# Performance work log

Measured on AMD Instinct MI355X. Metric: run time of the kernel, lower is better.

## Reference

```python
import jax, jax.numpy as jnp
import numpy as np

NEG_SLOPE = 0.2  # PyG GATConv default


def leaky_relu(v):
    return jnp.where(v >= 0, v, NEG_SLOPE * v)


def gat_conv(x, W, a_src, a_dst, b, src, dst, n_nodes):
    # x: [N, Fin], W: [Fin, Fout], a_src/a_dst/b: [Fout]
    h = x @ W                               # [N, Fout]
    alpha_src = h @ a_src                   # [N]
    alpha_dst = h @ a_dst                   # [N]
    e = leaky_relu(alpha_src[src] + alpha_dst[dst])          # [E]
    m = jax.ops.segment_max(e, dst, num_segments=n_nodes)    # [N] (self-loops => every node has >=1 edge)
    p = jnp.exp(e - m[dst])                                   # [E]
    s = jax.ops.segment_sum(p, dst, num_segments=n_nodes)     # [N]
    coef = p / s[dst]                                          # [E]
    out = jax.ops.segment_sum(coef[:, None] * h[src], dst, num_segments=n_nodes)
    return out + b


def setup_inputs() -> dict:
    key = jax.random.key(0)
    ks = jax.random.split(key, 20)
    N, E, DIN, DH, DOUT, G = 50000, 800000, 128, 256, 2, 512
    x = jax.random.normal(ks[0], (N, DIN), dtype=jnp.float32)
    edge_index = jax.random.randint(ks[1], (2, E), 0, N, dtype=jnp.int64)
    batch = jnp.sort(jax.random.randint(ks[2], (N,), 0, G, dtype=jnp.int64))

    def lin(k, fin, fout):
        return jax.random.normal(k, (fin, fout), dtype=jnp.float32) * (1.0 / np.sqrt(fin))

    def att(k, f):
        return jax.random.normal(k, (f,), dtype=jnp.float32) * (1.0 / np.sqrt(f))

    return {
        "x": x, "edge_index": edge_index, "batch": batch,
        "W1": lin(ks[3], DIN, DH), "as1": att(ks[4], DH), "ad1": att(ks[5], DH), "b1": jnp.zeros((DH,), jnp.float32),
        "W2": lin(ks[6], DH, DH),  "as2": att(ks[7], DH), "ad2": att(ks[8], DH), "b2": jnp.zeros((DH,), jnp.float32),
        "W3": lin(ks[9], DH, DH),  "as3": att(ks[10], DH), "ad3": att(ks[11], DH), "b3": jnp.zeros((DH,), jnp.float32),
        "Wfc": lin(ks[12], DH, DOUT), "bfc": jnp.zeros((DOUT,), jnp.float32),
    }


def reference(x, edge_index, batch, W1, as1, ad1, b1, W2, as2, ad2, b2, W3, as3, ad3, b3, Wfc, bfc):
    N = x.shape[0]
    G = 512  # number of graphs (static)
    # add self-loops (PyG GATConv default add_self_loops=True)
    loops = jnp.arange(N, dtype=edge_index.dtype)
    src = jnp.concatenate([edge_index[0], loops])
    dst = jnp.concatenate([edge_index[1], loops])

    h = jax.nn.relu(gat_conv(x, W1, as1, ad1, b1, src, dst, N))
    h = jax.nn.relu(gat_conv(h, W2, as2, ad2, b2, src, dst, N))
    h = jax.nn.relu(gat_conv(h, W3, as3, ad3, b3, src, dst, N))

    # global mean pool over graphs
    sums = jax.ops.segment_sum(h, batch, num_segments=G)                 # [G, DH]
    counts = jax.ops.segment_sum(jnp.ones((N,), h.dtype), batch, num_segments=G)
    pooled = sums / jnp.maximum(counts, 1.0)[:, None]

    logits = pooled @ Wfc + bfc                                           # [G, DOUT]
    return jax.nn.softmax(logits, axis=1)
```

## Files before the change

### kernel.cpp

```cpp
#include <hip/hip_runtime.h>
#include <hip/hip_bf16.h>

typedef short short8 __attribute__((ext_vector_type(8)));
typedef float floatx4 __attribute__((ext_vector_type(4)));
typedef unsigned short ushort_t;
typedef unsigned short ushort4v __attribute__((ext_vector_type(4)));

__device__ __forceinline__ ushort_t f2bf(float v) {
    __hip_bfloat16 h = __float2bfloat16(v);
    return *(ushort_t*)&h;
}
__device__ __forceinline__ float bf2f(ushort_t u) {
    return __uint_as_float(((unsigned)u) << 16);
}
__device__ __forceinline__ float4 ldh4(const ushort_t* p) {
    ushort4v u = *(const ushort4v*)p;
    return make_float4(bf2f(u.x), bf2f(u.y), bf2f(u.z), bf2f(u.w));
}

__global__ __launch_bounds__(256) void wsplit_kernel(const float* __restrict__ W,
                                                     ushort_t* __restrict__ Bthi,
                                                     ushort_t* __restrict__ Btlo, int K) {
    int idx = blockIdx.x * 256 + threadIdx.x;
    if (idx >= K * 256) return;
    int n = idx & 255, k = idx >> 8;
    float v = W[(size_t)k * 256 + n];
    ushort_t h = f2bf(v);
    float r = v - bf2f(h);
    Bthi[(size_t)n * K + k] = h;
    Btlo[(size_t)n * K + k] = f2bf(r);
}

#define ASTR 40
#define BSTR 56
__global__ __launch_bounds__(256, 2) void gemm_mfma(const float* __restrict__ A,
                                                    const ushort_t* __restrict__ Bthi,
                                                    const ushort_t* __restrict__ Btlo,
                                                    ushort_t* __restrict__ Hb,
                                                    const float* __restrict__ a_src,
                                                    const float* __restrict__ a_dst,
                                                    float* __restrict__ asrc_out,
                                                    float* __restrict__ adst_out,
                                                    int N, int K) {
    __shared__ ushort_t Ahi[128 * ASTR];
    __shared__ ushort_t Alo[128 * ASTR];
    __shared__ ushort_t Bhi[128 * BSTR];
    __shared__ ushort_t Blo[128 * BSTR];

    const int tid = threadIdx.x;
    const int wave = tid >> 6, lane = tid & 63;
    const int wr = wave & 1, wc = wave >> 1;
    const int q = lane >> 4, l15 = lane & 15;
    const int rowBase = blockIdx.x * 128;
    const int colBase = blockIdx.y * 128;

    floatx4 acc[4][4];
#pragma unroll
    for (int i = 0; i < 4; ++i)
#pragma unroll
        for (int j = 0; j < 4; ++j) acc[i][j] = (floatx4)0.f;

    const int a_row = tid >> 1;
    const int a_k0  = (tid & 1) * 16;
    const int b_n   = tid >> 1;
    const int b_k0  = (tid & 1) * 16;

    for (int kc = 0; kc < K; kc += 32) {
        {
            int grow = rowBase + a_row;
            float v[16];
            if (grow < N) {
                const float* ap = A + (size_t)grow * K + kc + a_k0;
                float4 t0 = *(const float4*)(ap + 0);
                float4 t1 = *(const float4*)(ap + 4);
                float4 t2 = *(const float4*)(ap + 8);
                float4 t3 = *(const float4*)(ap + 12);
                v[0]=t0.x; v[1]=t0.y; v[2]=t0.z; v[3]=t0.w;
                v[4]=t1.x; v[5]=t1.y; v[6]=t1.z; v[7]=t1.w;
                v[8]=t2.x; v[9]=t2.y; v[10]=t2.z; v[11]=t2.w;
                v[12]=t3.x; v[13]=t3.y; v[14]=t3.z; v[15]=t3.w;
            } else {
#pragma unroll
                for (int i = 0; i < 16; ++i) v[i] = 0.f;
            }
            int base = a_row * ASTR + a_k0;
#pragma unroll
            for (int i = 0; i < 16; i += 2) {
                ushort_t h0 = f2bf(v[i]),     h1 = f2bf(v[i + 1]);
                ushort_t l0 = f2bf(v[i] - bf2f(h0));
                ushort_t l1 = f2bf(v[i + 1] - bf2f(h1));
                *(uint*)&Ahi[base + i] = (uint)h0 | ((uint)h1 << 16);
                *(uint*)&Alo[base + i] = (uint)l0 | ((uint)l1 << 16);
            }
        }
        {
            const ushort_t* bh = Bthi + (size_t)(colBase + b_n) * K + kc + b_k0;
            const ushort_t* bl = Btlo + (size_t)(colBase + b_n) * K + kc + b_k0;
            int base = b_n * BSTR + b_k0;
            *(short8*)&Bhi[base + 0] = *(const short8*)(bh + 0);
            *(short8*)&Bhi[base + 8] = *(const short8*)(bh + 8);
            *(short8*)&Blo[base + 0] = *(const short8*)(bl + 0);
            *(short8*)&Blo[base + 8] = *(const short8*)(bl + 8);
        }
        __syncthreads();

        short8 afh[4], afl[4], bfh[4], bfl[4];
#pragma unroll
        for (int mt = 0; mt < 4; ++mt) {
            int r = wr * 64 + mt * 16 + l15;
            afh[mt] = *(short8*)&Ahi[r * ASTR + q * 8];
            afl[mt] = *(short8*)&Alo[r * ASTR + q * 8];
        }
#pragma unroll
        for (int nt = 0; nt < 4; ++nt) {
            int n = wc * 64 + nt * 16 + l15;
            bfh[nt] = *(short8*)&Bhi[n * BSTR + q * 8];
            bfl[nt] = *(short8*)&Blo[n * BSTR + q * 8];
        }
#pragma unroll
        for (int mt = 0; mt < 4; ++mt)
#pragma unroll
            for (int nt = 0; nt < 4; ++nt) {
                acc[mt][nt] = __builtin_amdgcn_mfma_f32_16x16x32_bf16(afh[mt], bfh[nt], acc[mt][nt], 0, 0, 0);
                acc[mt][nt] = __builtin_amdgcn_mfma_f32_16x16x32_bf16(afh[mt], bfl[nt], acc[mt][nt], 0, 0, 0);
                acc[mt][nt] = __builtin_amdgcn_mfma_f32_16x16x32_bf16(afl[mt], bfh[nt], acc[mt][nt], 0, 0, 0);
            }
        __syncthreads();
    }

    float asv[4], adv[4];
#pragma unroll
    for (int nt = 0; nt < 4; ++nt) {
        int n = colBase + wc * 64 + nt * 16 + l15;
        asv[nt] = a_src[n];
        adv[nt] = a_dst[n];
    }
#pragma unroll
    for (int mt = 0; mt < 4; ++mt) {
#pragma unroll
        for (int reg = 0; reg < 4; ++reg) {
            int grow = rowBase + wr * 64 + mt * 16 + q * 4 + reg;
            float p1 = acc[mt][0][reg] * asv[0] + acc[mt][1][reg] * asv[1] +
                       acc[mt][2][reg] * asv[2] + acc[mt][3][reg] * asv[3];
            float p2 = acc[mt][0][reg] * adv[0] + acc[mt][1][reg] * adv[1] +
                       acc[mt][2][reg] * adv[2] + acc[mt][3][reg] * adv[3];
            if (grow < N) {
                ushort_t* crow = Hb + (size_t)grow * 256 + colBase + wc * 64 + l15;
#pragma unroll
                for (int nt = 0; nt < 4; ++nt) crow[nt * 16] = f2bf(acc[mt][nt][reg]);
            }
#pragma unroll
            for (int off = 1; off < 16; off <<= 1) {
                p1 += __shfl_xor(p1, off, 64);
                p2 += __shfl_xor(p2, off, 64);
            }
            if (l15 == 0 && grow < N) {
                atomicAdd(&asrc_out[grow], p1);
                atomicAdd(&adst_out[grow], p2);
            }
        }
    }
}

__global__ __launch_bounds__(256) void count_kernel(const int* __restrict__ edst,
                                                    int* __restrict__ deg, int E) {
    int i = blockIdx.x * 256 + threadIdx.x;
    if (i < E) atomicAdd(&deg[edst[i]], 1);
}

__global__ __launch_bounds__(256) void scan1_kernel(const int* __restrict__ deg,
                                                    int* __restrict__ excl,
                                                    int* __restrict__ bsum, int N) {
    __shared__ int tmp[256];
    int tid = threadIdx.x;
    int i = blockIdx.x * 256 + tid;
    int v = (i < N) ? deg[i] : 0;
    tmp[tid] = v;
    __syncthreads();
    for (int off = 1; off < 256; off <<= 1) {
        int t = (tid >= off) ? tmp[tid - off] : 0;
        __syncthreads();
        tmp[tid] += t;
        __syncthreads();
    }
    if (i < N) excl[i] = tmp[tid] - v;
    if (tid == 255) bsum[blockIdx.x] = tmp[255];
}

__global__ __launch_bounds__(256) void scan2_kernel(int* __restrict__ bsum, int nb) {
    __shared__ int tmp[256];
    int tid = threadIdx.x;
    int v = (tid < nb) ? bsum[tid] : 0;
    tmp[tid] = v;
    __syncthreads();
    for (int off = 1; off < 256; off <<= 1) {
        int t = (tid >= off) ? tmp[tid - off] : 0;
        __syncthreads();
        tmp[tid] += t;
        __syncthreads();
    }
    if (tid < nb) bsum[tid] = tmp[tid] - v;
}

__global__ __launch_bounds__(256) void scan3_kernel(const int* __restrict__ excl,
                                                    const int* __restrict__ bsum,
                                                    int* __restrict__ rowptr,
                                                    int* __restrict__ cursor,
                                                    int N, int E) {
    int i = blockIdx.x * 256 + threadIdx.x;
    if (i < N) {
        int v = excl[i] + bsum[blockIdx.x];
        rowptr[i] = v;
        cursor[i] = v;
    }
    if (i == 0) rowptr[N] = E;
}

__global__ __launch_bounds__(256) void scatter_kernel(const int* __restrict__ esrc,
                                                      const int* __restrict__ edst,
                                                      int* __restrict__ cursor,
                                                      int* __restrict__ csr_src, int E) {
    int i = blockIdx.x * 256 + threadIdx.x;
    if (i < E) {
        int d = edst[i];
        int pos = atomicAdd(&cursor[d], 1);
        csr_src[pos] = esrc[i];
    }
}

__global__ __launch_bounds__(256) void gat_fused_kernel(const ushort_t* __restrict__ hb,
                                                        const float* __restrict__ asrc,
                                                        const float* __restrict__ adst,
                                                        const int* __restrict__ rowptr,
                                                        const int* __restrict__ csr_src,
                                                        const float* __restrict__ bias,
                                                        float* __restrict__ out, int N) {
    int wave = threadIdx.x >> 6;
    int lane = threadIdx.x & 63;
    int d = blockIdx.x * 4 + wave;
    if (d >= N) return;

    float ad = adst[d];
    float es = asrc[d] + ad;
    es = es >= 0.f ? es : 0.2f * es;
    float m = es;
    float s = 1.0f;
    float4 acc = ldh4(hb + (size_t)d * 256 + lane * 4);

    int beg = rowptr[d], end = rowptr[d + 1];
    for (int base = beg; base < end; base += 64) {
        int cnt = min(64, end - base);
        int srci = 0;
        float e = -1e30f;
        if (lane < cnt) {
            srci = csr_src[base + lane];
            float v = asrc[srci] + ad;
            e = v >= 0.f ? v : 0.2f * v;
        }
        float cm = e;
#pragma unroll
        for (int off = 32; off > 0; off >>= 1) cm = fmaxf(cm, __shfl_xor(cm, off, 64));
        float mnew = fmaxf(m, cm);
        float scale = __expf(m - mnew);
        s *= scale;
        acc.x *= scale; acc.y *= scale; acc.z *= scale; acc.w *= scale;
        m = mnew;

        int j = 0;
        for (; j + 4 <= cnt; j += 4) {
            float e0 = __shfl(e, j, 64),     e1 = __shfl(e, j + 1, 64);
            float e2 = __shfl(e, j + 2, 64), e3 = __shfl(e, j + 3, 64);
            int s0 = __shfl(srci, j, 64),     s1i = __shfl(srci, j + 1, 64);
            int s2i = __shfl(srci, j + 2, 64), s3i = __shfl(srci, j + 3, 64);
            float4 hv0 = ldh4(hb + (size_t)s0 * 256 + lane * 4);
            float4 hv1 = ldh4(hb + (size_t)s1i * 256 + lane * 4);
            float4 hv2 = ldh4(hb + (size_t)s2i * 256 + lane * 4);
            float4 hv3 = ldh4(hb + (size_t)s3i * 256 + lane * 4);
            float p0 = __expf(e0 - m), p1 = __expf(e1 - m);
            float p2 = __expf(e2 - m), p3 = __expf(e3 - m);
            s += p0 + p1 + p2 + p3;
            acc.x += p0 * hv0.x + p1 * hv1.x + p2 * hv2.x + p3 * hv3.x;
            acc.y += p0 * hv0.y + p1 * hv1.y + p2 * hv2.y + p3 * hv3.y;
            acc.z += p0 * hv0.z + p1 * hv1.z + p2 * hv2.z + p3 * hv3.z;
            acc.w += p0 * hv0.w + p1 * hv1.w + p2 * hv2.w + p3 * hv3.w;
        }
        for (; j < cnt; ++j) {
            float ej = __shfl(e, j, 64);
            int sj = __shfl(srci, j, 64);
            float p = __expf(ej - m);
            float4 hv = ldh4(hb + (size_t)sj * 256 + lane * 4);
            s += p;
            acc.x += p * hv.x; acc.y += p * hv.y; acc.z += p * hv.z; acc.w += p * hv.w;
        }
    }
    float inv = 1.0f / s;
    float4 bv = *(const float4*)(bias + lane * 4);
    float4 o;
    o.x = fmaxf(acc.x * inv + bv.x, 0.f);
    o.y = fmaxf(acc.y * inv + bv.y, 0.f);
    o.z = fmaxf(acc.z * inv + bv.z, 0.f);
    o.w = fmaxf(acc.w * inv + bv.w, 0.f);
    *(float4*)(out + (size_t)d * 256 + lane * 4) = o;
}

__device__ __forceinline__ int lower_bound_i(const int* __restrict__ a, int n, int v) {
    int lo = 0, hi = n;
    while (lo < hi) {
        int mid = (lo + hi) >> 1;
        if (a[mid] < v) lo = mid + 1; else hi = mid;
    }
    return lo;
}

__global__ __launch_bounds__(256) void pool_fc_kernel(const float* __restrict__ h,
                                                      const int* __restrict__ batch,
                                                      int N,
                                                      const float* __restrict__ Wfc,
                                                      const float* __restrict__ bfc,
                                                      float* __restrict__ out) {
    __shared__ float red0[256];
    __shared__ float red1[256];
    int g = blockIdx.x;
    int c = threadIdx.x;
    int beg = lower_bound_i(batch, N, g);
    int end = lower_bound_i(batch, N, g + 1);
    float sum = 0.f;
    for (int n = beg; n < end; ++n) sum += h[(size_t)n * 256 + c];
    float cnt = (float)(end - beg);
    float v = sum / fmaxf(cnt, 1.0f);
    red0[c] = v * Wfc[c * 2 + 0];
    red1[c] = v * Wfc[c * 2 + 1];
    __syncthreads();
    for (int off = 128; off > 0; off >>= 1) {
        if (c < off) {
            red0[c] += red0[c + off];
            red1[c] += red1[c + off];
        }
        __syncthreads();
    }
    if (c == 0) {
        float l0 = red0[0] + bfc[0];
        float l1 = red1[0] + bfc[1];
        float mx = fmaxf(l0, l1);
        float e0 = expf(l0 - mx), e1 = expf(l1 - mx);
        float s = e0 + e1;
        out[g * 2 + 0] = e0 / s;
        out[g * 2 + 1] = e1 / s;
    }
}

extern "C" void kernel_launch(void* const* d_in, const int* in_sizes, int n_in,
                              void* d_out, int out_size, void* d_ws, size_t ws_size,
                              hipStream_t stream) {
    const float* x    = (const float*)d_in[0];
    const int*   eidx = (const int*)d_in[1];
    const int*   batch= (const int*)d_in[2];
    const float* Wl[3]  = {(const float*)d_in[3], (const float*)d_in[7],  (const float*)d_in[11]};
    const float* asl[3] = {(const float*)d_in[4], (const float*)d_in[8],  (const float*)d_in[12]};
    const float* adl[3] = {(const float*)d_in[5], (const float*)d_in[9],  (const float*)d_in[13]};
    const float* bl[3]  = {(const float*)d_in[6], (const float*)d_in[10], (const float*)d_in[14]};
    const float* Wfc = (const float*)d_in[15];
    const float* bfc = (const float*)d_in[16];
    float* out = (float*)d_out;

    const int N  = in_sizes[2];
    const int E  = in_sizes[1] / 2;
    const int DH = 256;
    const int G  = 512;
    const int* esrc = eidx;
    const int* edst = eidx + E;

    char* ws = (char*)d_ws;
    size_t off = 0;
    const size_t featBytes = (size_t)N * DH * sizeof(float);
    ushort_t* hb     = (ushort_t*)(ws + off); off += (size_t)N * DH * sizeof(ushort_t);
    float*    bufB   = (float*)(ws + off); off += featBytes;
    float*    asrc   = (float*)(ws + off); off += (size_t)N * sizeof(float);
    float*    adst   = (float*)(ws + off); off += (size_t)N * sizeof(float);
    int*      deg    = (int*)(ws + off);   off += (size_t)N * sizeof(int);
    int*      excl   = (int*)(ws + off);   off += (size_t)N * sizeof(int);
    int*      rowptr = (int*)(ws + off);   off += (size_t)(N + 1) * sizeof(int);
    int*      cursor = (int*)(ws + off);   off += (size_t)N * sizeof(int);
    int*      bsum   = (int*)(ws + off);   off += 1024;
    int*      csrsrc = (int*)(ws + off);   off += (size_t)E * sizeof(int);
    ushort_t* Bthi   = (ushort_t*)(ws + off); off += (size_t)256 * 256 * sizeof(ushort_t);
    ushort_t* Btlo   = (ushort_t*)(ws + off); off += (size_t)256 * 256 * sizeof(ushort_t);

    const int nbN = (N + 255) / 256;

    hipMemsetAsync(deg, 0, (size_t)N * sizeof(int), stream);
    count_kernel<<<(E + 255) / 256, 256, 0, stream>>>(edst, deg, E);
    scan1_kernel<<<nbN, 256, 0, stream>>>(deg, excl, bsum, N);
    scan2_kernel<<<1, 256, 0, stream>>>(bsum, nbN);
    scan3_kernel<<<nbN, 256, 0, stream>>>(excl, bsum, rowptr, cursor, N, E);
    scatter_kernel<<<(E + 255) / 256, 256, 0, stream>>>(esrc, edst, cursor, csrsrc, E);

    for (int layer = 0; layer < 3; ++layer) {
        const float* in = (layer == 0) ? x : bufB;
        const int K = (layer == 0) ? 128 : 256;

        hipMemsetAsync(asrc, 0, 2 * (size_t)N * sizeof(float), stream);
        wsplit_kernel<<<K, 256, 0, stream>>>(Wl[layer], Bthi, Btlo, K);

        dim3 ggrid((N + 127) / 128, 2);
        gemm_mfma<<<ggrid, 256, 0, stream>>>(in, Bthi, Btlo, hb,
                                             asl[layer], adl[layer], asrc, adst, N, K);

        gat_fused_kernel<<<(N + 3) / 4, 256, 0, stream>>>(hb, asrc, adst, rowptr, csrsrc,
                                                          bl[layer], bufB, N);
    }

    pool_fc_kernel<<<G, 256, 0, stream>>>(bufB, batch, N, Wfc, bfc, out);
}
```

Measured before the change: 534.5 us.

## Pre-split activations into bf16 hi/lo planes outside the GEMM

The GAT aggregation kernel now writes its output directly as bf16 hi/lo pairs, and a new pre-pass splits x the same way, so the GEMM loads ready-made hi/lo tiles instead of converting fp32 per tile. LDS padding is unified to a single stride and the occupancy hint is raised to 4 blocks per CU. Pooling reads and sums the two planes. This removes conversion ALU work from the GEMM inner loop while keeping the same bytes per feature. The cost is an extra split kernel and a possible LDS bank-conflict change from the new stride.

```diff
diff --git a/kernel.cpp b/kernel.cpp
--- a/kernel.cpp
+++ b/kernel.cpp
@@ -16,6 +16,17 @@
 __device__ __forceinline__ float4 ldh4(const ushort_t* p) {
     ushort4v u = *(const ushort4v*)p;
     return make_float4(bf2f(u.x), bf2f(u.y), bf2f(u.z), bf2f(u.w));
+}
+
+__global__ __launch_bounds__(256) void xsplit_kernel(const float* __restrict__ X,
+                                                     ushort_t* __restrict__ Xhi,
+                                                     ushort_t* __restrict__ Xlo, int total) {
+    int idx = blockIdx.x * 256 + threadIdx.x;
+    if (idx >= total) return;
+    float v = X[idx];
+    ushort_t h = f2bf(v);
+    Xhi[idx] = h;
+    Xlo[idx] = f2bf(v - bf2f(h));
 }
 
 __global__ __launch_bounds__(256) void wsplit_kernel(const float* __restrict__ W,
@@ -31,9 +42,9 @@
     Btlo[(size_t)n * K + k] = f2bf(r);
 }
 
-#define ASTR 40
-#define BSTR 56
-__global__ __launch_bounds__(256, 2) void gemm_mfma(const float* __restrict__ A,
+#define LSTR 36
+__global__ __launch_bounds__(256, 4) void gemm_mfma(const ushort_t* __restrict__ Ahi_g,
+                                                    const ushort_t* __restrict__ Alo_g,
                                                     const ushort_t* __restrict__ Bthi,
                                                     const ushort_t* __restrict__ Btlo,
                                                     ushort_t* __restrict__ Hb,
@@ -42,10 +53,10 @@
                                                     float* __restrict__ asrc_out,
                                                     float* __restrict__ adst_out,
                                                     int N, int K) {
-    __shared__ ushort_t Ahi[128 * ASTR];
-    __shared__ ushort_t Alo[128 * ASTR];
-    __shared__ ushort_t Bhi[128 * BSTR];
-    __shared__ ushort_t Blo[128 * BSTR];
+    __shared__ ushort_t Ahi[128 * LSTR];
+    __shared__ ushort_t Alo[128 * LSTR];
+    __shared__ ushort_t Bhi[128 * LSTR];
+    __shared__ ushort_t Blo[128 * LSTR];
 
     const int tid = threadIdx.x;
     const int wave = tid >> 6, lane = tid & 63;
@@ -62,41 +73,30 @@
 
     const int a_row = tid >> 1;
     const int a_k0  = (tid & 1) * 16;
-    const int b_n   = tid >> 1;
-    const int b_k0  = (tid & 1) * 16;
+    const short8 zero8 = (short8)0;
 
     for (int kc = 0; kc < K; kc += 32) {
         {
             int grow = rowBase + a_row;
-            float v[16];
+            int base = a_row * LSTR + a_k0;
             if (grow < N) {
-                const float* ap = A + (size_t)grow * K + kc + a_k0;
-                float4 t0 = *(const float4*)(ap + 0);
-                float4 t1 = *(const float4*)(ap + 4);
-                float4 t2 = *(const float4*)(ap + 8);
-                float4 t3 = *(const float4*)(ap + 12);
-                v[0]=t0.x; v[1]=t0.y; v[2]=t0.z; v[3]=t0.w;
-                v[4]=t1.x; v[5]=t1.y; v[6]=t1.z; v[7]=t1.w;
-                v[8]=t2.x; v[9]=t2.y; v[10]=t2.z; v[11]=t2.w;
-                v[12]=t3.x; v[13]=t3.y; v[14]=t3.z; v[15]=t3.w;
+                const ushort_t* ah = Ahi_g + (size_t)grow * K + kc + a_k0;
+                const ushort_t* al = Alo_g + (size_t)grow * K + kc + a_k0;
+                *(short8*)&Ahi[base + 0] = *(const short8*)(ah + 0);
+                *(short8*)&Ahi[base + 8] = *(const short8*)(ah + 8);
+                *(short8*)&Alo[base + 0] = *(const short8*)(al + 0);
+                *(short8*)&Alo[base + 8] = *(const short8*)(al + 8);
             } else {
-#pragma unroll
-                for (int i = 0; i < 16; ++i) v[i] = 0.f;
+                *(short8*)&Ahi[base + 0] = zero8;
+                *(short8*)&Ahi[base + 8] = zero8;
+                *(short8*)&Alo[base + 0] = zero8;
+                *(short8*)&Alo[base + 8] = zero8;
             }
-            int base = a_row * ASTR + a_k0;
-#pragma unroll
-            for (int i = 0; i < 16; i += 2) {
-                ushort_t h0 = f2bf(v[i]),     h1 = f2bf(v[i + 1]);
-                ushort_t l0 = f2bf(v[i] - bf2f(h0));
-                ushort_t l1 = f2bf(v[i + 1] - bf2f(h1));
-                *(uint*)&Ahi[base + i] = (uint)h0 | ((uint)h1 << 16);
-                *(uint*)&Alo[base + i] = (uint)l0 | ((uint)l1 << 16);
-            }
         }
         {
-            const ushort_t* bh = Bthi + (size_t)(colBase + b_n) * K + kc + b_k0;
-            const ushort_t* bl = Btlo + (size_t)(colBase + b_n) * K + kc + b_k0;
-            int base = b_n * BSTR + b_k0;
+            const ushort_t* bh = Bthi + (size_t)(colBase + a_row) * K + kc + a_k0;
+            const ushort_t* bl = Btlo + (size_t)(colBase + a_row) * K + kc + a_k0;
+            int base = a_row * LSTR + a_k0;
             *(short8*)&Bhi[base + 0] = *(const short8*)(bh + 0);
             *(short8*)&Bhi[base + 8] = *(const short8*)(bh + 8);
             *(short8*)&Blo[base + 0] = *(const short8*)(bl + 0);
@@ -108,14 +108,14 @@
 #pragma unroll
         for (int mt = 0; mt < 4; ++mt) {
             int r = wr * 64 + mt * 16 + l15;
-            afh[mt] = *(short8*)&Ahi[r * ASTR + q * 8];
-            afl[mt] = *(short8*)&Alo[r * ASTR + q * 8];
+            afh[mt] = *(short8*)&Ahi[r * LSTR + q * 8];
+            afl[mt] = *(short8*)&Alo[r * LSTR + q * 8];
         }
 #pragma unroll
         for (int nt = 0; nt < 4; ++nt) {
             int n = wc * 64 + nt * 16 + l15;
-            bfh[nt] = *(short8*)&Bhi[n * BSTR + q * 8];
-            bfl[nt] = *(short8*)&Blo[n * BSTR + q * 8];
+            bfh[nt] = *(short8*)&Bhi[n * LSTR + q * 8];
+            bfl[nt] = *(short8*)&Blo[n * LSTR + q * 8];
         }
 #pragma unroll
         for (int mt = 0; mt < 4; ++mt)
@@ -234,7 +234,8 @@
                                                         const int* __restrict__ rowptr,
                                                         const int* __restrict__ csr_src,
                                                         const float* __restrict__ bias,
-                                                        float* __restrict__ out, int N) {
+                                                        ushort_t* __restrict__ ohi,
+                                                        ushort_t* __restrict__ olo, int N) {
     int wave = threadIdx.x >> 6;
     int lane = threadIdx.x & 63;
     int d = blockIdx.x * 4 + wave;
@@ -295,12 +296,17 @@
     }
     float inv = 1.0f / s;
     float4 bv = *(const float4*)(bias + lane * 4);
-    float4 o;
-    o.x = fmaxf(acc.x * inv + bv.x, 0.f);
-    o.y = fmaxf(acc.y * inv + bv.y, 0.f);
-    o.z = fmaxf(acc.z * inv + bv.z, 0.f);
-    o.w = fmaxf(acc.w * inv + bv.w, 0.f);
-    *(float4*)(out + (size_t)d * 256 + lane * 4) = o;
+    float ox = fmaxf(acc.x * inv + bv.x, 0.f);
+    float oy = fmaxf(acc.y * inv + bv.y, 0.f);
+    float oz = fmaxf(acc.z * inv + bv.z, 0.f);
+    float ow = fmaxf(acc.w * inv + bv.w, 0.f);
+    ushort4v hv, lv;
+    hv.x = f2bf(ox); lv.x = f2bf(ox - bf2f(hv.x));
+    hv.y = f2bf(oy); lv.y = f2bf(oy - bf2f(hv.y));
+    hv.z = f2bf(oz); lv.z = f2bf(oz - bf2f(hv.z));
+    hv.w = f2bf(ow); lv.w = f2bf(ow - bf2f(hv.w));
+    *(ushort4v*)(ohi + (size_t)d * 256 + lane * 4) = hv;
+    *(ushort4v*)(olo + (size_t)d * 256 + lane * 4) = lv;
 }
 
 __device__ __forceinline__ int lower_bound_i(const int* __restrict__ a, int n, int v) {
@@ -312,7 +318,8 @@
     return lo;
 }
 
-__global__ __launch_bounds__(256) void pool_fc_kernel(const float* __restrict__ h,
+__global__ __launch_bounds__(256) void pool_fc_kernel(const ushort_t* __restrict__ hhi,
+                                                      const ushort_t* __restrict__ hlo,
                                                       const int* __restrict__ batch,
                                                       int N,
                                                       const float* __restrict__ Wfc,
@@ -325,7 +332,8 @@
     int beg = lower_bound_i(batch, N, g);
     int end = lower_bound_i(batch, N, g + 1);
     float sum = 0.f;
-    for (int n = beg; n < end; ++n) sum += h[(size_t)n * 256 + c];
+    for (int n = beg; n < end; ++n)
+        sum += bf2f(hhi[(size_t)n * 256 + c]) + bf2f(hlo[(size_t)n * 256 + c]);
     float cnt = (float)(end - beg);
     float v = sum / fmaxf(cnt, 1.0f);
     red0[c] = v * Wfc[c * 2 + 0];
@@ -363,18 +371,22 @@
     const float* bfc = (const float*)d_in[16];
     float* out = (float*)d_out;
 
-    const int N  = in_sizes[2];
-    const int E  = in_sizes[1] / 2;
-    const int DH = 256;
-    const int G  = 512;
+    const int N   = in_sizes[2];
+    const int E   = in_sizes[1] / 2;
+    const int DIN = in_sizes[0] / N;
+    const int DH  = 256;
+    const int G   = 512;
     const int* esrc = eidx;
     const int* edst = eidx + E;
 
     char* ws = (char*)d_ws;
     size_t off = 0;
-    const size_t featBytes = (size_t)N * DH * sizeof(float);
-    ushort_t* hb     = (ushort_t*)(ws + off); off += (size_t)N * DH * sizeof(ushort_t);
-    float*    bufB   = (float*)(ws + off); off += featBytes;
+    const size_t featHalf = (size_t)N * DH * sizeof(ushort_t);
+    ushort_t* hb     = (ushort_t*)(ws + off); off += featHalf;
+    ushort_t* ghi    = (ushort_t*)(ws + off); off += featHalf;
+    ushort_t* glo    = (ushort_t*)(ws + off); off += featHalf;
+    ushort_t* xhi    = (ushort_t*)(ws + off); off += (size_t)N * DIN * sizeof(ushort_t);
+    ushort_t* xlo    = (ushort_t*)(ws + off); off += (size_t)N * DIN * sizeof(ushort_t);
     float*    asrc   = (float*)(ws + off); off += (size_t)N * sizeof(float);
     float*    adst   = (float*)(ws + off); off += (size_t)N * sizeof(float);
     int*      deg    = (int*)(ws + off);   off += (size_t)N * sizeof(int);
@@ -395,20 +407,23 @@
     scan3_kernel<<<nbN, 256, 0, stream>>>(excl, bsum, rowptr, cursor, N, E);
     scatter_kernel<<<(E + 255) / 256, 256, 0, stream>>>(esrc, edst, cursor, csrsrc, E);
 
+    xsplit_kernel<<<((size_t)N * DIN + 255) / 256, 256, 0, stream>>>(x, xhi, xlo, N * DIN);
+
     for (int layer = 0; layer < 3; ++layer) {
-        const float* in = (layer == 0) ? x : bufB;
-        const int K = (layer == 0) ? 128 : 256;
+        const ushort_t* Ah = (layer == 0) ? xhi : ghi;
+        const ushort_t* Al = (layer == 0) ? xlo : glo;
+        const int K = (layer == 0) ? DIN : DH;
 
         hipMemsetAsync(asrc, 0, 2 * (size_t)N * sizeof(float), stream);
         wsplit_kernel<<<K, 256, 0, stream>>>(Wl[layer], Bthi, Btlo, K);
 
         dim3 ggrid((N + 127) / 128, 2);
-        gemm_mfma<<<ggrid, 256, 0, stream>>>(in, Bthi, Btlo, hb,
+        gemm_mfma<<<ggrid, 256, 0, stream>>>(Ah, Al, Bthi, Btlo, hb,
                                              asl[layer], adl[layer], asrc, adst, N, K);
 
         gat_fused_kernel<<<(N + 3) / 4, 256, 0, stream>>>(hb, asrc, adst, rowptr, csrsrc,
-                                                          bl[layer], bufB, N);
-    }
-
-    pool_fc_kernel<<<G, 256, 0, stream>>>(bufB, batch, N, Wfc, bfc, out);
-}
+                                                          bl[layer], ghi, glo, N);
+    }
+
+    pool_fc_kernel<<<G, 256, 0, stream>>>(ghi, glo, batch, N, Wfc, bfc, out);
+}
```

Result: slower. 552.2 us (+3.3%).
